# Performance work log

Measured on AMD Instinct MI355X. Metric: run time of the kernel, lower is better.

## Reference

```python
import jax, jax.numpy as jnp
import numpy as np

# Module hyper-parameters (init_kwargs)
CLIPVAR = 5.0   # variance is clipped to this before confidence = exp(-var)
MAXRANGE = 16   # max integration radius (pixels) in each of 4 directions
LAM = 0.05      # blend factor between depthin and CRF lateral estimate
N_CLASSES = 19


def _shift(x, axis, d, fill):
    """d=+1: out[..., n] = x[..., n-1] (pad with fill); d=-1: out[..., n] = x[..., n+1]."""
    pad = [(0, 0)] * x.ndim
    idx = [slice(None)] * x.ndim
    L = x.shape[axis]
    if d > 0:
        pad[axis] = (1, 0)
        idx[axis] = slice(0, L)
    else:
        pad[axis] = (0, 1)
        idx[axis] = slice(1, L + 1)
    return jnp.pad(x, pad, constant_values=fill)[tuple(idx)]


def _dir_accum(g, sem, msk, var, dep, axis, d, pre_shift, sign, clipvar, R):
    """Accumulate confidence-weighted depth estimates propagated from up to R
    same-semantic neighbors along one direction. All arrays are [bz,h,w].
    Depth estimate from neighbor at offset s: dep[neighbor] * exp(signed path
    sum of log-gradients g along the traversal)."""
    zeros = jnp.zeros_like(dep)
    valid0 = (msk == 1)  # only masked centers receive contributions

    def step(carry, _):
        g_sh, sem_sh, msk_sh, var_sh, dep_sh, pathlog, valid, dsum, csum = carry
        if pre_shift:  # newly added gradient term lives at the neighbor pixel
            g_sh = _shift(g_sh, axis, d, 0.0)
            pathlog = pathlog + sign * g_sh
        else:          # newly added gradient term lives one step before neighbor
            pathlog = pathlog + sign * g_sh
            g_sh = _shift(g_sh, axis, d, 0.0)
        sem_sh = _shift(sem_sh, axis, d, -1)
        msk_sh = _shift(msk_sh, axis, d, 0)
        var_sh = _shift(var_sh, axis, d, 0.0)
        dep_sh = _shift(dep_sh, axis, d, 0.0)
        # traversal stops (stays stopped) at semantic boundary / invalid pixel
        valid = valid & (sem_sh == sem) & (msk_sh == 1)
        conf = jnp.where(valid, jnp.exp(-jnp.minimum(var_sh, clipvar)), 0.0)
        dsum = dsum + conf * dep_sh * jnp.exp(pathlog)
        csum = csum + conf
        return (g_sh, sem_sh, msk_sh, var_sh, dep_sh, pathlog, valid, dsum, csum), None

    carry0 = (g, sem, msk, var, dep, zeros, valid0, zeros, zeros)
    carry, _ = jax.lax.scan(step, carry0, None, length=R)
    return carry[-2], carry[-1]


def crf_integrate(pred_log, semantics, mask, variance, depthin, clipvar, R):
    g0 = pred_log[:, 0]  # horizontal log-gradient: log d[n+1] - log d[n]
    g1 = pred_log[:, 1]  # vertical   log-gradient: log d[m+1] - log d[m]
    sem = semantics[:, 0]
    msk = mask[:, 0]
    var = variance[:, 0]
    dep = depthin[:, 0]
    # self term
    selfconf = jnp.where(msk == 1, jnp.exp(-jnp.minimum(var, clipvar)), 0.0)
    dsum = selfconf * dep
    csum = selfconf
    # (gradient map, axis, shift dir, pre_shift_g, sign): left, right, up, down
    dirs = [(g0, 2, 1, True, 1.0), (g0, 2, -1, False, -1.0),
            (g1, 1, 1, True, 1.0), (g1, 1, -1, False, -1.0)]
    for g, axis, d, pre, sgn in dirs:
        ds, cs = _dir_accum(g, sem, msk, var, dep, axis, d, pre, sgn, clipvar, R)
        dsum = dsum + ds
        csum = csum + cs
    out = jnp.where(csum > 0, dsum / jnp.maximum(csum, 1e-12), 0.0)
    return out[:, None]  # [bz,1,h,w]


def setup_inputs() -> dict:
    key = jax.random.key(0)
    k1, k2, k3, k4, k5 = jax.random.split(key, 5)
    bz, h, w = 4, 256, 832
    pred_log = 0.1 * jax.random.normal(k1, (bz, 2, h, w), dtype=jnp.float32)
    semantics = jax.random.randint(k2, (bz, 1, h, w), 0, N_CLASSES, dtype=jnp.int32)
    mask = jax.random.randint(k3, (bz, 1, h, w), 0, 2, dtype=jnp.int32)
    variance = 5.0 * jax.random.uniform(k4, (bz, 1, h, w), dtype=jnp.float32)
    depthin = 0.5 + 10.0 * jax.random.uniform(k5, (bz, 1, h, w), dtype=jnp.float32)
    return {"pred_log": pred_log, "semantics": semantics, "mask": mask,
            "variance": variance, "depthin": depthin, "times": 1}


def reference(pred_log, semantics, mask, variance, depthin, times):
    depthout = depthin
    for _ in range(times):
        lateral = crf_integrate(pred_log, semantics, mask, variance, depthout,
                                 CLIPVAR, MAXRANGE)
        sel = (lateral > 0).astype(depthin.dtype)
        depthout = (1.0 - sel) * depthin + sel * (depthin * LAM + lateral * (1.0 - LAM))
    return depthout
```

## Files before the change

### kernel.cpp

```cpp
#include <hip/hip_runtime.h>

#define W 832
#define H 256
#define BZ 4
#define RR 16
#define LAM_C 0.05f

#define CT 32
#define S  64
#define NT 512
#define NBLK (26 * 8 * 4)


__device__ __forceinline__ unsigned bf16r(float x) {
    const unsigned u = __float_as_uint(x);
    return (u + 0x7FFFu + ((u >> 16) & 1u)) >> 16;
}
__device__ __forceinline__ float decDep(unsigned p) {
    return __uint_as_float(p & 0xFFFF0000u);
}
__device__ __forceinline__ float decCF(unsigned p) {
    return __uint_as_float(0x3B800000u + ((p & 0xFFE0u) << 11));
}

__global__ __launch_bounds__(NT) void k_fused(
    const float* __restrict__ pred_log, const int* __restrict__ sem,
    const int* __restrict__ msk, const float* __restrict__ var,
    const float* __restrict__ dep, float* __restrict__ out)
{
    __shared__ unsigned sP1[S * S];

    const int orig = blockIdx.x;
    const int wg   = (orig & 7) * 104 + (orig >> 3);
    const int bz   = wg / 208;
    const int rem  = wg - bz * 208;
    const int by   = rem / 26;
    const int bx   = rem - by * 26;

    const int tid = threadIdx.x;
    const int c0 = bx * CT;
    const int r0 = by * CT;
    const int im0 = bz * (H * W);
    const float* g0p = pred_log + (size_t)(bz * 2) * (H * W);
    const float* g1p = pred_log + (size_t)(bz * 2 + 1) * (H * W);

    const int cr0 = tid >> 5;
    const int col = tid & 31;
    const int c   = c0 + col;
    const int ra = r0 + cr0, rb = ra + 16;
    const int rWa = ra * W, rWb = rb * W;
    float4 h0a, h0b;
    if (c >= 2 && c <= W - 2) {
        h0a = *reinterpret_cast<const float4*>(&g0p[rWa + c - 2]);
        h0b = *reinterpret_cast<const float4*>(&g0p[rWb + c - 2]);
    } else {
        h0a.x = g0p[rWa + max(c - 2, 0)]; h0a.y = g0p[rWa + max(c - 1, 0)];
        h0a.z = g0p[rWa + c];             h0a.w = g0p[rWa + min(c + 1, W - 1)];
        h0b.x = g0p[rWb + max(c - 2, 0)]; h0b.y = g0p[rWb + max(c - 1, 0)];
        h0b.z = g0p[rWb + c];             h0b.w = g0p[rWb + min(c + 1, W - 1)];
    }
    const float u2a = g1p[max(ra - 2, 0) * W + c];
    const float u1a = g1p[max(ra - 1, 0) * W + c];
    const float d1a = g1p[rWa + c];
    const float d2a = g1p[min(ra + 1, H - 1) * W + c];
    const float u2b = g1p[max(rb - 2, 0) * W + c];
    const float u1b = g1p[max(rb - 1, 0) * W + c];
    const float d1b = g1p[rWb + c];
    const float d2b = g1p[min(rb + 1, H - 1) * W + c];

    #pragma unroll
    for (int k = 0; k < 2; ++k) {
        const int q = tid + NT * k;
        const int sr = q >> 4;
        const int sc4 = (q & 15) << 2;
        const int rimg = r0 - RR + sr;
        const int cimg = c0 - RR + sc4;
        const bool corner = ((sr < RR) || (sr >= RR + CT)) &&
                            ((sc4 < RR) || (sc4 >= RR + CT));
        uint4 p4 = make_uint4(31u, 31u, 31u, 31u);
        if (!corner && (unsigned)rimg < H && (unsigned)cimg < W) {
            const int off = im0 + rimg * W + cimg;
            const int4   mk4 = *reinterpret_cast<const int4*>(&msk[off]);
            const int4   se4 = *reinterpret_cast<const int4*>(&sem[off]);
            const float4 vr4 = *reinterpret_cast<const float4*>(&var[off]);
            const float4 dp4 = *reinterpret_cast<const float4*>(&dep[off]);
            #pragma unroll
            for (int e = 0; e < 4; ++e) {
                unsigned w = bf16r((&dp4.x)[e]) << 16;
                if ((&mk4.x)[e] == 1) {
                    const float cf = __expf(-fminf((&vr4.x)[e], 5.f));
                    const unsigned enc =
                        (__float_as_uint(cf) - 0x3B800000u + 0x8000u) >> 16;
                    w |= (enc << 5) | (unsigned)(&se4.x)[e];
                } else w |= 31u;
                (&p4.x)[e] = w;
            }
        }
        *reinterpret_cast<uint4*>(&sP1[sr * S + sc4]) = p4;
    }
    __syncthreads();

    #pragma unroll
    for (int j = 0; j < 2; ++j) {
        const int cr = cr0 + 16 * j;
        const int r  = r0 + cr;
        const int rW = r * W;
        const int ci = (cr + RR) * S + RR + col;
        const float4 h0 = j ? h0b : h0a;
        const float gU2 = j ? u2b : u2a, gU1 = j ? u1b : u1a;
        const float gD1 = j ? d1b : d1a, gD2 = j ? d2b : d2a;

        const unsigned uc = sP1[ci];
        const unsigned semc = uc & 31u;
        const bool alive = (semc != 31u);

        const unsigned uL1 = sP1[ci - 1],     uL2 = sP1[ci - 2];
        const unsigned uR1 = sP1[ci + 1],     uR2 = sP1[ci + 2];
        const unsigned uU1 = sP1[ci - S],     uU2 = sP1[ci - 2 * S];
        const unsigned uD1 = sP1[ci + S],     uD2 = sP1[ci + 2 * S];

        const bool vL1 = alive && ((uL1 & 31u) == semc);
        const bool vR1 = alive && ((uR1 & 31u) == semc);
        const bool vU1 = alive && ((uU1 & 31u) == semc);
        const bool vD1 = alive && ((uD1 & 31u) == semc);
        const bool vL2 = vL1 && ((uL2 & 31u) == semc);
        const bool vR2 = vR1 && ((uR2 & 31u) == semc);
        const bool vU2 = vU1 && ((uU2 & 31u) == semc);
        const bool vD2 = vD1 && ((uD2 & 31u) == semc);

        const float cfc = decCF(uc);
        float ds = alive ? cfc * decDep(uc) : 0.0f;
        float cs = alive ? cfc : 0.0f;

        const float pL2 = h0.y + h0.x, pR2 = -h0.z - h0.w;
        const float pU2 = gU1 + gU2,   pD2 = -gD1 - gD2;

        ds = fmaf(vL1 ? decCF(uL1) * decDep(uL1) : 0.f, __expf(h0.y),  ds);
        cs += vL1 ? decCF(uL1) : 0.f;
        ds = fmaf(vL2 ? decCF(uL2) * decDep(uL2) : 0.f, __expf(pL2),   ds);
        cs += vL2 ? decCF(uL2) : 0.f;
        ds = fmaf(vR1 ? decCF(uR1) * decDep(uR1) : 0.f, __expf(-h0.z), ds);
        cs += vR1 ? decCF(uR1) : 0.f;
        ds = fmaf(vR2 ? decCF(uR2) * decDep(uR2) : 0.f, __expf(pR2),   ds);
        cs += vR2 ? decCF(uR2) : 0.f;
        ds = fmaf(vU1 ? decCF(uU1) * decDep(uU1) : 0.f, __expf(gU1),   ds);
        cs += vU1 ? decCF(uU1) : 0.f;
        ds = fmaf(vU2 ? decCF(uU2) * decDep(uU2) : 0.f, __expf(pU2),   ds);
        cs += vU2 ? decCF(uU2) : 0.f;
        ds = fmaf(vD1 ? decCF(uD1) * decDep(uD1) : 0.f, __expf(-gD1),  ds);
        cs += vD1 ? decCF(uD1) : 0.f;
        ds = fmaf(vD2 ? decCF(uD2) * decDep(uD2) : 0.f, __expf(pD2),   ds);
        cs += vD2 ? decCF(uD2) : 0.f;

        if (vL2) {
            float psum = pL2;
            #pragma unroll 1
            for (int s = 3; s <= RR; ++s) {
                const unsigned u = sP1[ci - s];
                if ((u & 31u) != semc) break;
                psum += g0p[rW + (c - s)];
                ds = fmaf(decCF(u) * decDep(u), __expf(psum), ds);
                cs += decCF(u);
            }
        }
        if (vR2) {
            float psum = pR2;
            #pragma unroll 1
            for (int s = 3; s <= RR; ++s) {
                const unsigned u = sP1[ci + s];
                if ((u & 31u) != semc) break;
                psum -= g0p[rW + (c + s - 1)];
                ds = fmaf(decCF(u) * decDep(u), __expf(psum), ds);
                cs += decCF(u);
            }
        }
        if (vU2) {
            float psum = pU2;
            #pragma unroll 1
            for (int s = 3; s <= RR; ++s) {
                const unsigned u = sP1[ci - s * S];
                if ((u & 31u) != semc) break;
                psum += g1p[(r - s) * W + c];
                ds = fmaf(decCF(u) * decDep(u), __expf(psum), ds);
                cs += decCF(u);
            }
        }
        if (vD2) {
            float psum = pD2;
            #pragma unroll 1
            for (int s = 3; s <= RR; ++s) {
                const unsigned u = sP1[ci + s * S];
                if ((u & 31u) != semc) break;
                psum -= g1p[(r + s - 1) * W + c];
                ds = fmaf(decCF(u) * decDep(u), __expf(psum), ds);
                cs += decCF(u);
            }
        }

        const float dpin = decDep(uc);
        const float lat = (cs > 0.0f) ? (ds / fmaxf(cs, 1e-12f)) : 0.0f;
        out[im0 + rW + c] =
            (lat > 0.0f) ? fmaf(lat, 1.0f - LAM_C, dpin * LAM_C) : dpin;
    }
}

extern "C" void kernel_launch(void* const* d_in, const int* in_sizes, int n_in,
                              void* d_out, int out_size, void* d_ws, size_t ws_size,
                              hipStream_t stream)
{
    const float* pred_log = (const float*)d_in[0];
    const int*   sem      = (const int*)d_in[1];
    const int*   msk      = (const int*)d_in[2];
    const float* var      = (const float*)d_in[3];
    const float* dep      = (const float*)d_in[4];

    float* out = (float*)d_out;

    hipLaunchKernelGGL(k_fused, dim3(NBLK), dim3(NT), 0, stream,
                       pred_log, sem, msk, var, dep, out);
}
```

Baseline: 13.68 us.

## Shrink shared-memory halo to 2 pixels and read long-range neighbors from global

The shared-memory tile shrinks from a 64x64 halo of 16 pixels to 36x40, covering only the 2-pixel neighborhood used by the unrolled near terms. Walks past distance 2, which are rare with random semantics and masks, now read mask, semantics, variance and depth straight from global memory and recompute confidence. This cuts the staging loads, packing work and LDS footprint, which may also allow more blocks per CU. The cost is scattered uncached global reads and full-precision depth instead of bf16 on the rare long walks.

```diff
diff --git a/kernel.cpp b/kernel.cpp
--- a/kernel.cpp
+++ b/kernel.cpp
@@ -7,7 +7,8 @@
 #define LAM_C 0.05f
 
 #define CT 32
-#define S  64
+#define SSW 40
+#define SSH 36
 #define NT 512
 #define NBLK (26 * 8 * 4)
 
@@ -28,7 +29,7 @@
     const int* __restrict__ msk, const float* __restrict__ var,
     const float* __restrict__ dep, float* __restrict__ out)
 {
-    __shared__ unsigned sP1[S * S];
+    __shared__ unsigned sP1[SSH * SSW];
 
     const int orig = blockIdx.x;
     const int wg   = (orig & 7) * 104 + (orig >> 3);
@@ -68,17 +69,13 @@
     const float d1b = g1p[rWb + c];
     const float d2b = g1p[min(rb + 1, H - 1) * W + c];
 
-    #pragma unroll
-    for (int k = 0; k < 2; ++k) {
-        const int q = tid + NT * k;
-        const int sr = q >> 4;
-        const int sc4 = (q & 15) << 2;
-        const int rimg = r0 - RR + sr;
-        const int cimg = c0 - RR + sc4;
-        const bool corner = ((sr < RR) || (sr >= RR + CT)) &&
-                            ((sc4 < RR) || (sc4 >= RR + CT));
+    if (tid < SSH * (SSW / 4)) {
+        const int sr  = tid / (SSW / 4);
+        const int sc4 = (tid - sr * (SSW / 4)) * 4;
+        const int rimg = r0 - 2 + sr;
+        const int cimg = c0 - 4 + sc4;
         uint4 p4 = make_uint4(31u, 31u, 31u, 31u);
-        if (!corner && (unsigned)rimg < H && (unsigned)cimg < W) {
+        if ((unsigned)rimg < H && (unsigned)cimg < W) {
             const int off = im0 + rimg * W + cimg;
             const int4   mk4 = *reinterpret_cast<const int4*>(&msk[off]);
             const int4   se4 = *reinterpret_cast<const int4*>(&sem[off]);
@@ -96,7 +93,7 @@
                 (&p4.x)[e] = w;
             }
         }
-        *reinterpret_cast<uint4*>(&sP1[sr * S + sc4]) = p4;
+        *reinterpret_cast<uint4*>(&sP1[sr * SSW + sc4]) = p4;
     }
     __syncthreads();
 
@@ -105,7 +102,7 @@
         const int cr = cr0 + 16 * j;
         const int r  = r0 + cr;
         const int rW = r * W;
-        const int ci = (cr + RR) * S + RR + col;
+        const int ci = (cr + 2) * SSW + 4 + col;
         const float4 h0 = j ? h0b : h0a;
         const float gU2 = j ? u2b : u2a, gU1 = j ? u1b : u1a;
         const float gD1 = j ? d1b : d1a, gD2 = j ? d2b : d2a;
@@ -114,10 +111,10 @@
         const unsigned semc = uc & 31u;
         const bool alive = (semc != 31u);
 
-        const unsigned uL1 = sP1[ci - 1],     uL2 = sP1[ci - 2];
-        const unsigned uR1 = sP1[ci + 1],     uR2 = sP1[ci + 2];
-        const unsigned uU1 = sP1[ci - S],     uU2 = sP1[ci - 2 * S];
-        const unsigned uD1 = sP1[ci + S],     uD2 = sP1[ci + 2 * S];
+        const unsigned uL1 = sP1[ci - 1],       uL2 = sP1[ci - 2];
+        const unsigned uR1 = sP1[ci + 1],       uR2 = sP1[ci + 2];
+        const unsigned uU1 = sP1[ci - SSW],     uU2 = sP1[ci - 2 * SSW];
+        const unsigned uD1 = sP1[ci + SSW],     uD2 = sP1[ci + 2 * SSW];
 
         const bool vL1 = alive && ((uL1 & 31u) == semc);
         const bool vR1 = alive && ((uR1 & 31u) == semc);
@@ -156,44 +153,56 @@
             float psum = pL2;
             #pragma unroll 1
             for (int s = 3; s <= RR; ++s) {
-                const unsigned u = sP1[ci - s];
-                if ((u & 31u) != semc) break;
-                psum += g0p[rW + (c - s)];
-                ds = fmaf(decCF(u) * decDep(u), __expf(psum), ds);
-                cs += decCF(u);
+                const int cc2 = c - s;
+                if (cc2 < 0) break;
+                const int off = im0 + rW + cc2;
+                if (msk[off] != 1 || (unsigned)sem[off] != semc) break;
+                psum += g0p[rW + cc2];
+                const float cf = __expf(-fminf(var[off], 5.f));
+                ds = fmaf(cf * dep[off], __expf(psum), ds);
+                cs += cf;
             }
         }
         if (vR2) {
             float psum = pR2;
             #pragma unroll 1
             for (int s = 3; s <= RR; ++s) {
-                const unsigned u = sP1[ci + s];
-                if ((u & 31u) != semc) break;
-                psum -= g0p[rW + (c + s - 1)];
-                ds = fmaf(decCF(u) * decDep(u), __expf(psum), ds);
-                cs += decCF(u);
+                const int cc2 = c + s;
+                if (cc2 >= W) break;
+                const int off = im0 + rW + cc2;
+                if (msk[off] != 1 || (unsigned)sem[off] != semc) break;
+                psum -= g0p[rW + cc2 - 1];
+                const float cf = __expf(-fminf(var[off], 5.f));
+                ds = fmaf(cf * dep[off], __expf(psum), ds);
+                cs += cf;
             }
         }
         if (vU2) {
             float psum = pU2;
             #pragma unroll 1
             for (int s = 3; s <= RR; ++s) {
-                const unsigned u = sP1[ci - s * S];
-                if ((u & 31u) != semc) break;
-                psum += g1p[(r - s) * W + c];
-                ds = fmaf(decCF(u) * decDep(u), __expf(psum), ds);
-                cs += decCF(u);
+                const int rr2 = r - s;
+                if (rr2 < 0) break;
+                const int off = im0 + rr2 * W + c;
+                if (msk[off] != 1 || (unsigned)sem[off] != semc) break;
+                psum += g1p[rr2 * W + c];
+                const float cf = __expf(-fminf(var[off], 5.f));
+                ds = fmaf(cf * dep[off], __expf(psum), ds);
+                cs += cf;
             }
         }
         if (vD2) {
             float psum = pD2;
             #pragma unroll 1
             for (int s = 3; s <= RR; ++s) {
-                const unsigned u = sP1[ci + s * S];
-                if ((u & 31u) != semc) break;
-                psum -= g1p[(r + s - 1) * W + c];
-                ds = fmaf(decCF(u) * decDep(u), __expf(psum), ds);
-                cs += decCF(u);
+                const int rr2 = r + s;
+                if (rr2 >= H) break;
+                const int off = im0 + rr2 * W + c;
+                if (msk[off] != 1 || (unsigned)sem[off] != semc) break;
+                psum -= g1p[(rr2 - 1) * W + c];
+                const float cf = __expf(-fminf(var[off], 5.f));
+                ds = fmaf(cf * dep[off], __expf(psum), ds);
+                cs += cf;
             }
         }
 
```

After: 12.48 us. 1.1x faster.
